# Kernel tuning notes

Hardware: AMD Instinct MI355X
Metric: run time of the kernel (lower is better)

Reference implementation:

```python
import jax, jax.numpy as jnp
import numpy as np

WS = 16  # window_size
C1 = (0.01 * 255.0) ** 2
C2 = (0.03 * 255.0) ** 2


def _box(img):
    # Faithful to F.conv2d(img, ones(1,C,ws,ws)/ws^2, stride=ws):
    # sums over channels AND window, divides by ws^2 only.
    b, c, h, w = img.shape
    blk = img.reshape(b, c, h // WS, WS, w // WS, WS)
    return blk.sum(axis=(1, 3, 5)) / (WS * WS)  # (b, h//WS, w//WS)


def setup_inputs() -> dict:
    key = jax.random.key(0)
    k1, k2 = jax.random.split(key)
    x = jax.random.uniform(k1, (32, 3, 512, 512), dtype=jnp.float32)
    y = jax.random.uniform(k2, (32, 3, 512, 512), dtype=jnp.float32)
    return {"x": x, "y": y}


def reference(x, y):
    mean_x = _box(x)
    mean_y = _box(y)
    mean_x_sq = mean_x ** 2
    mean_y_sq = mean_y ** 2
    var_x = _box(x * x) - mean_x_sq
    var_y = _box(y * y) - mean_y_sq
    cov_xy = _box(x * y) - mean_x * mean_y
    num = (2.0 * mean_x * mean_y + C1) * (2.0 * cov_xy + C2)
    den = (mean_x_sq + mean_y_sq + C1) * (var_x + var_y + C2)
    ssim = (num / den).mean(axis=(1, 2))  # conv out had channel dim 1; mean over (1,2,3) == mean over spatial blocks
    return (1.0 - ssim) / 2.0  # shape (b,)
```

## Files before the change

kernel.cpp:

```cpp
#include <hip/hip_runtime.h>
#include <hip/hip_bf16.h>

#define WS 16
#define C1 6.5025f
#define C2 58.5225f

__global__ __launch_bounds__(256) void ssim_stage1(
    const float* __restrict__ x, const float* __restrict__ y,
    float* __restrict__ partial)
{
    const int wg  = blockIdx.x;
    const int b   = wg >> 5;
    const int bh  = wg & 31;
    const int tid = threadIdx.x;
    const int h_local = tid >> 7;
    const int w4 = tid & 127;
    const int w  = w4 << 2;
    const int bw = w >> 4;

    float sx = 0.f, sy = 0.f, sxx = 0.f, syy = 0.f, sxy = 0.f;

    const size_t batch_off = (size_t)b * 3u * 512u * 512u;
    const int h0 = bh * WS + h_local;

    #pragma unroll
    for (int c = 0; c < 3; ++c) {
        #pragma unroll
        for (int hp = 0; hp < 8; ++hp) {
            const int h = h0 + hp * 2;
            const size_t off = batch_off + ((size_t)c * 512u + (size_t)h) * 512u + (size_t)w;
            const float4 xv = *reinterpret_cast<const float4*>(x + off);
            const float4 yv = *reinterpret_cast<const float4*>(y + off);
            sx += (xv.x + xv.y) + (xv.z + xv.w);
            sy += (yv.x + yv.y) + (yv.z + yv.w);
            sxx = fmaf(xv.x, xv.x, sxx); sxx = fmaf(xv.y, xv.y, sxx);
            sxx = fmaf(xv.z, xv.z, sxx); sxx = fmaf(xv.w, xv.w, sxx);
            syy = fmaf(yv.x, yv.x, syy); syy = fmaf(yv.y, yv.y, syy);
            syy = fmaf(yv.z, yv.z, syy); syy = fmaf(yv.w, yv.w, syy);
            sxy = fmaf(xv.x, yv.x, sxy); sxy = fmaf(xv.y, yv.y, sxy);
            sxy = fmaf(xv.z, yv.z, sxy); sxy = fmaf(xv.w, yv.w, sxy);
        }
    }

    #pragma unroll
    for (int d = 1; d < 4; d <<= 1) {
        sx  += __shfl_xor(sx,  d);
        sy  += __shfl_xor(sy,  d);
        sxx += __shfl_xor(sxx, d);
        syy += __shfl_xor(syy, d);
        sxy += __shfl_xor(sxy, d);
    }

    __shared__ float sums[2][32][5];
    if ((tid & 3) == 0) {
        sums[h_local][bw][0] = sx;
        sums[h_local][bw][1] = sy;
        sums[h_local][bw][2] = sxx;
        sums[h_local][bw][3] = syy;
        sums[h_local][bw][4] = sxy;
    }
    __syncthreads();

    if (tid < 32) {
        const float Sx  = sums[0][tid][0] + sums[1][tid][0];
        const float Sy  = sums[0][tid][1] + sums[1][tid][1];
        const float Sxx = sums[0][tid][2] + sums[1][tid][2];
        const float Syy = sums[0][tid][3] + sums[1][tid][3];
        const float Sxy = sums[0][tid][4] + sums[1][tid][4];

        const float inv = 1.0f / 256.0f;
        const float mx  = Sx * inv;
        const float my  = Sy * inv;
        const float mx2 = mx * mx;
        const float my2 = my * my;
        const float vx  = Sxx * inv - mx2;
        const float vy  = Syy * inv - my2;
        const float cxy = Sxy * inv - mx * my;

        const float num  = (2.0f * mx * my + C1) * (2.0f * cxy + C2);
        const float den  = (mx2 + my2 + C1) * (vx + vy + C2);
        float ssim = num / den;

        #pragma unroll
        for (int d = 1; d < 32; d <<= 1) ssim += __shfl_xor(ssim, d);
        if (tid == 0) partial[wg] = ssim;
    }
}

__global__ __launch_bounds__(64) void ssim_stage2(
    const float* __restrict__ partial, float* __restrict__ out)
{
    const int b = blockIdx.x;
    const int lane = threadIdx.x;
    float v = (lane < 32) ? partial[b * 32 + lane] : 0.f;
    #pragma unroll
    for (int d = 1; d < 64; d <<= 1) v += __shfl_xor(v, d);
    if (lane == 0) {
        const float mean_ssim = v * (1.0f / 1024.0f);
        out[b] = (1.0f - mean_ssim) * 0.5f;
    }
}

extern "C" void kernel_launch(void* const* d_in, const int* in_sizes, int n_in,
                              void* d_out, int out_size, void* d_ws, size_t ws_size,
                              hipStream_t stream) {
    const float* x = (const float*)d_in[0];
    const float* y = (const float*)d_in[1];
    float* out = (float*)d_out;
    float* partial = (float*)d_ws;

    ssim_stage1<<<1024, 256, 0, stream>>>(x, y, partial);
    ssim_stage2<<<32, 64, 0, stream>>>(partial, out);
}
```

Before: 212.4 us.

## Split stage1 work per wave over channel/half-window rows with software-pipelined loads

Measured after the change: 218.1 us. +2.7%, slower.

```diff
diff --git a/kernel.cpp b/kernel.cpp
--- a/kernel.cpp
+++ b/kernel.cpp
@@ -1,72 +1,120 @@
 #include <hip/hip_runtime.h>
 #include <hip/hip_bf16.h>
 
-#define WS 16
 #define C1 6.5025f
 #define C2 58.5225f
 
 __global__ __launch_bounds__(256) void ssim_stage1(
     const float* __restrict__ x, const float* __restrict__ y,
-    float* __restrict__ partial)
+    float* __restrict__ ws)
 {
-    const int wg  = blockIdx.x;
-    const int b   = wg >> 5;
-    const int bh  = wg & 31;
-    const int tid = threadIdx.x;
-    const int h_local = tid >> 7;
-    const int w4 = tid & 127;
-    const int w  = w4 << 2;
-    const int bw = w >> 4;
+    const int tid  = threadIdx.x;
+    const int lane = tid & 63;
+    const int W    = blockIdx.x * 4 + (tid >> 6);
 
-    float sx = 0.f, sy = 0.f, sxx = 0.f, syy = 0.f, sxy = 0.f;
+    const int hg = W & 1;
+    const int t1 = W >> 1;
+    const int c  = t1 % 3;
+    const int br = t1 / 3;
+    const int b  = br >> 5;
+    const int bh = br & 31;
+    const int h0 = bh * 16 + hg * 8;
 
-    const size_t batch_off = (size_t)b * 3u * 512u * 512u;
-    const int h0 = bh * WS + h_local;
+    const size_t row0 = (((size_t)(b * 3 + c)) * 512 + (size_t)h0) * 512;
+    const float* px = x + row0 + (size_t)(lane * 4);
+    const float* py = y + row0 + (size_t)(lane * 4);
 
-    #pragma unroll
-    for (int c = 0; c < 3; ++c) {
-        #pragma unroll
-        for (int hp = 0; hp < 8; ++hp) {
-            const int h = h0 + hp * 2;
-            const size_t off = batch_off + ((size_t)c * 512u + (size_t)h) * 512u + (size_t)w;
-            const float4 xv = *reinterpret_cast<const float4*>(x + off);
-            const float4 yv = *reinterpret_cast<const float4*>(y + off);
-            sx += (xv.x + xv.y) + (xv.z + xv.w);
-            sy += (yv.x + yv.y) + (yv.z + yv.w);
-            sxx = fmaf(xv.x, xv.x, sxx); sxx = fmaf(xv.y, xv.y, sxx);
-            sxx = fmaf(xv.z, xv.z, sxx); sxx = fmaf(xv.w, xv.w, sxx);
-            syy = fmaf(yv.x, yv.x, syy); syy = fmaf(yv.y, yv.y, syy);
-            syy = fmaf(yv.z, yv.z, syy); syy = fmaf(yv.w, yv.w, syy);
-            sxy = fmaf(xv.x, yv.x, sxy); sxy = fmaf(xv.y, yv.y, sxy);
-            sxy = fmaf(xv.z, yv.z, sxy); sxy = fmaf(xv.w, yv.w, sxy);
-        }
-    }
+    float s0x = 0.f, s0y = 0.f, s0xx = 0.f, s0yy = 0.f, s0xy = 0.f;
+    float s1x = 0.f, s1y = 0.f, s1xx = 0.f, s1yy = 0.f, s1xy = 0.f;
+
+#define LOADR(XA, XB, YA, YB, r)                                   \
+    XA = *reinterpret_cast<const float4*>(px + (r) * 512);         \
+    XB = *reinterpret_cast<const float4*>(px + (r) * 512 + 256);   \
+    YA = *reinterpret_cast<const float4*>(py + (r) * 512);         \
+    YB = *reinterpret_cast<const float4*>(py + (r) * 512 + 256);
+
+#define CONSUME(XA, XB, YA, YB)                                        \
+    s0x += (XA.x + XA.y) + (XA.z + XA.w);                              \
+    s0y += (YA.x + YA.y) + (YA.z + YA.w);                              \
+    s0xx = fmaf(XA.x, XA.x, s0xx); s0xx = fmaf(XA.y, XA.y, s0xx);      \
+    s0xx = fmaf(XA.z, XA.z, s0xx); s0xx = fmaf(XA.w, XA.w, s0xx);      \
+    s0yy = fmaf(YA.x, YA.x, s0yy); s0yy = fmaf(YA.y, YA.y, s0yy);      \
+    s0yy = fmaf(YA.z, YA.z, s0yy); s0yy = fmaf(YA.w, YA.w, s0yy);      \
+    s0xy = fmaf(XA.x, YA.x, s0xy); s0xy = fmaf(XA.y, YA.y, s0xy);      \
+    s0xy = fmaf(XA.z, YA.z, s0xy); s0xy = fmaf(XA.w, YA.w, s0xy);      \
+    s1x += (XB.x + XB.y) + (XB.z + XB.w);                              \
+    s1y += (YB.x + YB.y) + (YB.z + YB.w);                              \
+    s1xx = fmaf(XB.x, XB.x, s1xx); s1xx = fmaf(XB.y, XB.y, s1xx);      \
+    s1xx = fmaf(XB.z, XB.z, s1xx); s1xx = fmaf(XB.w, XB.w, s1xx);      \
+    s1yy = fmaf(YB.x, YB.x, s1yy); s1yy = fmaf(YB.y, YB.y, s1yy);      \
+    s1yy = fmaf(YB.z, YB.z, s1yy); s1yy = fmaf(YB.w, YB.w, s1yy);      \
+    s1xy = fmaf(XB.x, YB.x, s1xy); s1xy = fmaf(XB.y, YB.y, s1xy);      \
+    s1xy = fmaf(XB.z, YB.z, s1xy); s1xy = fmaf(XB.w, YB.w, s1xy);
+
+    float4 xa0, xa1, ya0, ya1;
+    float4 xb0, xb1, yb0, yb1;
+
+    LOADR(xa0, xa1, ya0, ya1, 0)
+    LOADR(xb0, xb1, yb0, yb1, 1)
+    CONSUME(xa0, xa1, ya0, ya1)
+    LOADR(xa0, xa1, ya0, ya1, 2)
+    CONSUME(xb0, xb1, yb0, yb1)
+    LOADR(xb0, xb1, yb0, yb1, 3)
+    CONSUME(xa0, xa1, ya0, ya1)
+    LOADR(xa0, xa1, ya0, ya1, 4)
+    CONSUME(xb0, xb1, yb0, yb1)
+    LOADR(xb0, xb1, yb0, yb1, 5)
+    CONSUME(xa0, xa1, ya0, ya1)
+    LOADR(xa0, xa1, ya0, ya1, 6)
+    CONSUME(xb0, xb1, yb0, yb1)
+    LOADR(xb0, xb1, yb0, yb1, 7)
+    CONSUME(xa0, xa1, ya0, ya1)
+    CONSUME(xb0, xb1, yb0, yb1)
+#undef LOADR
+#undef CONSUME
 
     #pragma unroll
     for (int d = 1; d < 4; d <<= 1) {
-        sx  += __shfl_xor(sx,  d);
-        sy  += __shfl_xor(sy,  d);
-        sxx += __shfl_xor(sxx, d);
-        syy += __shfl_xor(syy, d);
-        sxy += __shfl_xor(sxy, d);
+        s0x  += __shfl_xor(s0x,  d); s0y  += __shfl_xor(s0y,  d);
+        s0xx += __shfl_xor(s0xx, d); s0yy += __shfl_xor(s0yy, d);
+        s0xy += __shfl_xor(s0xy, d);
+        s1x  += __shfl_xor(s1x,  d); s1y  += __shfl_xor(s1y,  d);
+        s1xx += __shfl_xor(s1xx, d); s1yy += __shfl_xor(s1yy, d);
+        s1xy += __shfl_xor(s1xy, d);
     }
 
-    __shared__ float sums[2][32][5];
-    if ((tid & 3) == 0) {
-        sums[h_local][bw][0] = sx;
-        sums[h_local][bw][1] = sy;
-        sums[h_local][bw][2] = sxx;
-        sums[h_local][bw][3] = syy;
-        sums[h_local][bw][4] = sxy;
+    if ((lane & 3) == 0) {
+        const int bw0 = lane >> 2;
+        float* p0 = ws + (size_t)W * 160 + bw0 * 5;
+        p0[0] = s0x; p0[1] = s0y; p0[2] = s0xx; p0[3] = s0yy; p0[4] = s0xy;
+        float* p1 = p0 + 80;
+        p1[0] = s1x; p1[1] = s1y; p1[2] = s1xx; p1[3] = s1yy; p1[4] = s1xy;
     }
-    __syncthreads();
+}
 
-    if (tid < 32) {
-        const float Sx  = sums[0][tid][0] + sums[1][tid][0];
-        const float Sy  = sums[0][tid][1] + sums[1][tid][1];
-        const float Sxx = sums[0][tid][2] + sums[1][tid][2];
-        const float Syy = sums[0][tid][3] + sums[1][tid][3];
-        const float Sxy = sums[0][tid][4] + sums[1][tid][4];
+__global__ __launch_bounds__(256) void ssim_stage2(
+    const float* __restrict__ ws, float* __restrict__ out)
+{
+    const int b   = blockIdx.x;
+    const int tid = threadIdx.x;
+
+    float acc = 0.f;
+    #pragma unroll
+    for (int k = 0; k < 4; ++k) {
+        const int blk = tid * 4 + k;
+        const int bh  = blk >> 5;
+        const int bw  = blk & 31;
+
+        float Sx = 0.f, Sy = 0.f, Sxx = 0.f, Syy = 0.f, Sxy = 0.f;
+        #pragma unroll
+        for (int c = 0; c < 3; ++c) {
+            #pragma unroll
+            for (int hg = 0; hg < 2; ++hg) {
+                const int W = ((b * 32 + bh) * 3 + c) * 2 + hg;
+                const float* p = ws + (size_t)W * 160 + bw * 5;
+                Sx += p[0]; Sy += p[1]; Sxx += p[2]; Syy += p[3]; Sxy += p[4];
+            }
+        }
 
         const float inv = 1.0f / 256.0f;
         const float mx  = Sx * inv;
@@ -77,27 +125,20 @@
         const float vy  = Syy * inv - my2;
         const float cxy = Sxy * inv - mx * my;
 
-        const float num  = (2.0f * mx * my + C1) * (2.0f * cxy + C2);
-        const float den  = (mx2 + my2 + C1) * (vx + vy + C2);
-        float ssim = num / den;
+        const float num = (2.0f * mx * my + C1) * (2.0f * cxy + C2);
+        const float den = (mx2 + my2 + C1) * (vx + vy + C2);
+        acc += num / den;
+    }
 
-        #pragma unroll
-        for (int d = 1; d < 32; d <<= 1) ssim += __shfl_xor(ssim, d);
-        if (tid == 0) partial[wg] = ssim;
-    }
-}
+    #pragma unroll
+    for (int d = 1; d < 64; d <<= 1) acc += __shfl_xor(acc, d);
 
-__global__ __launch_bounds__(64) void ssim_stage2(
-    const float* __restrict__ partial, float* __restrict__ out)
-{
-    const int b = blockIdx.x;
-    const int lane = threadIdx.x;
-    float v = (lane < 32) ? partial[b * 32 + lane] : 0.f;
-    #pragma unroll
-    for (int d = 1; d < 64; d <<= 1) v += __shfl_xor(v, d);
-    if (lane == 0) {
-        const float mean_ssim = v * (1.0f / 1024.0f);
-        out[b] = (1.0f - mean_ssim) * 0.5f;
+    __shared__ float red[4];
+    if ((tid & 63) == 0) red[tid >> 6] = acc;
+    __syncthreads();
+    if (tid == 0) {
+        const float total = (red[0] + red[1]) + (red[2] + red[3]);
+        out[b] = (1.0f - total * (1.0f / 1024.0f)) * 0.5f;
     }
 }
 
@@ -107,8 +148,8 @@
     const float* x = (const float*)d_in[0];
     const float* y = (const float*)d_in[1];
     float* out = (float*)d_out;
-    float* partial = (float*)d_ws;
+    float* ws  = (float*)d_ws;
 
-    ssim_stage1<<<1024, 256, 0, stream>>>(x, y, partial);
-    ssim_stage2<<<32, 64, 0, stream>>>(partial, out);
+    ssim_stage1<<<1536, 256, 0, stream>>>(x, y, ws);
+    ssim_stage2<<<32, 256, 0, stream>>>(ws, out);
 }
```
